# Kernel optimization log

Hardware: AMD Instinct MI355X
Metric: run time of the kernel (lower is better)

## Reference

```python
import jax, jax.numpy as jnp
import numpy as np

MAX_DEGREE = 7  # selected_degree for every neuron (== config.max_degree)


def _cheb_combine(alpha, coeffs):
    """sum_d coeffs[:, d] * T_d(alpha) via the Chebyshev recurrence.

    alpha:  [B, out]
    coeffs: [out, D+1]
    returns [B, out]
    """
    t_m2 = jnp.ones_like(alpha)          # T_0
    t_m1 = alpha                          # T_1
    acc = coeffs[:, 0] + coeffs[:, 1] * alpha

    def body(carry, c_d):                 # c_d: [out]
        tm2, tm1, a = carry
        t = 2.0 * alpha * tm1 - tm2       # T_d recurrence
        return (tm1, t, a + c_d * t), None

    (_, _, acc), _ = jax.lax.scan(body, (t_m2, t_m1, acc), coeffs[:, 2:].T)
    return acc


def _kan_layer(x, w, b, coeffs, cW, cb):
    # w: [out, in] (stacked per-neuron projection vectors), b: [out]
    alpha = x @ w.T + b                   # [B, out] -- per-neuron scalar projection
    neuron_out = _cheb_combine(alpha, coeffs)  # [B, out]
    return neuron_out @ cW + cb           # combine_W [out,out], combin_b [out]


def setup_inputs() -> dict:
    key = jax.random.key(0)
    ks = jax.random.split(key, 12)
    B = 16384
    shape = [1024, 1024, 256]
    D1 = MAX_DEGREE + 1
    inp = {"x": jax.random.normal(ks[0], (B, shape[0]), dtype=jnp.float32)}
    ki = 1
    for li, (din, dout) in enumerate(zip(shape[:-1], shape[1:]), start=1):
        inp[f"w{li}"] = jax.random.normal(ks[ki], (dout, din), dtype=jnp.float32) / np.sqrt(din); ki += 1
        inp[f"b{li}"] = jnp.zeros((dout,), dtype=jnp.float32)
        inp[f"coeffs{li}"] = jax.random.normal(ks[ki], (dout, D1), dtype=jnp.float32) * 0.1; ki += 1
        inp[f"cW{li}"] = jnp.eye(dout, dtype=jnp.float32)
        inp[f"cb{li}"] = jnp.zeros((dout,), dtype=jnp.float32)
    return inp


def reference(x, w1, b1, coeffs1, cW1, cb1, w2, b2, coeffs2, cW2, cb2):
    h = _kan_layer(x, w1, b1, coeffs1, cW1, cb1)
    return _kan_layer(h, w2, b2, coeffs2, cW2, cb2)
```

## Files before the change

kernel.cpp:

```cpp
#include <hip/hip_runtime.h>


typedef __attribute__((ext_vector_type(8))) short short8;
typedef __attribute__((ext_vector_type(4))) float f32x4;
typedef unsigned short ushort_t;

#define GAS(p) ((const __attribute__((address_space(1))) void*)(p))
#define LAS(p) ((__attribute__((address_space(3))) void*)(p))

__device__ __forceinline__ void split2(float f, ushort_t& h, ushort_t& l) {
    const unsigned u = __float_as_uint(f);
    h = (ushort_t)(u >> 16);
    const float hf = __uint_as_float(u & 0xFFFF0000u);
    l = (ushort_t)(__float_as_uint(f - hf) >> 16);
}

__global__ __launch_bounds__(256) void split_f32(const float* __restrict__ src,
                                                 ushort_t* __restrict__ hi,
                                                 ushort_t* __restrict__ lo, int n4) {
    const int i = blockIdx.x * 256 + threadIdx.x;
    if (i >= n4) return;
    const float4 v = ((const float4*)src)[i];
    ushort4 h, l;
    split2(v.x, h.x, l.x); split2(v.y, h.y, l.y);
    split2(v.z, h.z, l.z); split2(v.w, h.w, l.w);
    ((ushort4*)hi)[i] = h;
    ((ushort4*)lo)[i] = l;
}

__global__ __launch_bounds__(256) void bias2eff_kernel(const float* __restrict__ cb1,
                                                       const float* __restrict__ w2,
                                                       const float* __restrict__ b2,
                                                       float* __restrict__ out) {
    const int n = threadIdx.x;
    float s = 0.f;
    for (int k = 0; k < 1024; ++k) s = fmaf(cb1[k], w2[n * 1024 + k], s);
    out[n] = s + b2[n];
}

__global__ __launch_bounds__(256) void tsplit_kernel(const float* __restrict__ src,
                                                     ushort_t* __restrict__ hiT,
                                                     ushort_t* __restrict__ loT) {
    const int i = blockIdx.x * 256 + threadIdx.x;
    const int r = i >> 8, c = i & 255;
    ushort_t h, l;
    split2(src[r * 256 + c], h, l);
    hiT[c * 256 + r] = h;
    loT[c * 256 + r] = l;
}

constexpr int PKT = 16;
__global__ __launch_bounds__(256)
void prep_gemm_sk(const float* __restrict__ A, const float* __restrict__ W,
                  float* __restrict__ Cp, int M, int N, int K, int KS) {
    __shared__ float As[PKT][68];
    __shared__ float Bs[PKT][68];
    const int tid = threadIdx.x;
    const int bn = blockIdx.x, bm = blockIdx.y, bz = blockIdx.z;
    const int kc = K / KS, k0 = bz * kc;
    const int tx = tid & 15, ty = tid >> 4;
    float acc[4][4];
#pragma unroll
    for (int i = 0; i < 4; ++i)
#pragma unroll
        for (int j = 0; j < 4; ++j) acc[i][j] = 0.f;
    const float* Ab = A + (size_t)(bm * 64) * K + k0;
    const float* Wb = W + (size_t)(bn * 64) * K + k0;
    const int sr = tid >> 2;
    const int sc = (tid & 3) * 4;
    for (int kt = 0; kt < kc; kt += PKT) {
        const float4 va = *(const float4*)(Ab + (size_t)sr * K + kt + sc);
        As[sc + 0][sr] = va.x; As[sc + 1][sr] = va.y; As[sc + 2][sr] = va.z; As[sc + 3][sr] = va.w;
        const float4 vb = *(const float4*)(Wb + (size_t)sr * K + kt + sc);
        Bs[sc + 0][sr] = vb.x; Bs[sc + 1][sr] = vb.y; Bs[sc + 2][sr] = vb.z; Bs[sc + 3][sr] = vb.w;
        __syncthreads();
#pragma unroll
        for (int k = 0; k < PKT; ++k) {
            const float4 a4 = *(const float4*)&As[k][ty * 4];
            const float4 b4 = *(const float4*)&Bs[k][tx * 4];
            const float a[4] = {a4.x, a4.y, a4.z, a4.w};
            const float b[4] = {b4.x, b4.y, b4.z, b4.w};
#pragma unroll
            for (int i = 0; i < 4; ++i)
#pragma unroll
                for (int j = 0; j < 4; ++j) acc[i][j] = fmaf(a[i], b[j], acc[i][j]);
        }
        __syncthreads();
    }
    float* Cb = Cp + (size_t)bz * M * N + (size_t)(bm * 64 + ty * 4) * N + bn * 64 + tx * 4;
#pragma unroll
    for (int i = 0; i < 4; ++i)
        *(float4*)(Cb + (size_t)i * N) = make_float4(acc[i][0], acc[i][1], acc[i][2], acc[i][3]);
}

__global__ __launch_bounds__(256)
void combine_split(const float* __restrict__ Cp, ushort_t* __restrict__ hi,
                   ushort_t* __restrict__ lo, int n4, int KS) {
    const int i = blockIdx.x * 256 + threadIdx.x;
    if (i >= n4) return;
    float4 s = ((const float4*)Cp)[i];
    for (int z = 1; z < KS; ++z) {
        const float4 v = ((const float4*)Cp)[(size_t)z * n4 + i];
        s.x += v.x; s.y += v.y; s.z += v.z; s.w += v.w;
    }
    ushort4 h, l;
    split2(s.x, h.x, l.x); split2(s.y, h.y, l.y);
    split2(s.z, h.z, l.z); split2(s.w, h.w, l.w);
    ((ushort4*)hi)[i] = h;
    ((ushort4*)lo)[i] = l;
}

template<bool CHEB, bool OUT_F32>
__global__ __launch_bounds__(256)
void kan_mfma(const ushort_t* __restrict__ Ahg,
              const ushort_t* __restrict__ Alg,
              const ushort_t* __restrict__ Bhg,
              const ushort_t* __restrict__ Blg,
              const float* __restrict__ bias,
              const float* __restrict__ coeffs,
              float* __restrict__ Cf,
              ushort_t* __restrict__ Chh,
              ushort_t* __restrict__ Chl,
              int M, int N, int K)
{
    __shared__ __align__(16) ushort_t Ah[128 * 32];
    __shared__ __align__(16) ushort_t Al[128 * 32];
    __shared__ __align__(16) ushort_t Bh[128 * 32];
    __shared__ __align__(16) ushort_t Bl[128 * 32];

    const int tid  = threadIdx.x;
    const int lane = tid & 63;
    const int wave = tid >> 6;

    const int gx = gridDim.x;
    const int nwg = gx * gridDim.y;
    int wg = blockIdx.y * gx + blockIdx.x;
    wg = (wg & 7) * (nwg >> 3) + (wg >> 3);
    const int bn = wg % gx;
    const int bm = wg / gx;

    const int wm = wave >> 1, wn = wave & 1;
    const int lr = lane & 15;
    const int lg = lane >> 4;

    f32x4 acc[4][4];
#pragma unroll
    for (int m = 0; m < 4; ++m)
#pragma unroll
        for (int n = 0; n < 4; ++n) acc[m][n] = f32x4{0.f, 0.f, 0.f, 0.f};

    const size_t aRow0 = (size_t)(bm * 128);
    const size_t bRow0 = (size_t)(bn * 128);
    const int g = wave;
    const int ldsb = g * 1024;

    for (int kt = 0; kt < K; kt += 32) {
#pragma unroll
        for (int r0 = 0; r0 < 128; r0 += 64) {
            const size_t goA = (aRow0 + r0 + lane) * K + kt + g * 8;
            const size_t goB = (bRow0 + r0 + lane) * K + kt + g * 8;
            __builtin_amdgcn_global_load_lds(GAS(Ahg + goA), LAS(&Ah[ldsb + r0 * 8]), 16, 0, 0);
            __builtin_amdgcn_global_load_lds(GAS(Alg + goA), LAS(&Al[ldsb + r0 * 8]), 16, 0, 0);
            __builtin_amdgcn_global_load_lds(GAS(Bhg + goB), LAS(&Bh[ldsb + r0 * 8]), 16, 0, 0);
            __builtin_amdgcn_global_load_lds(GAS(Blg + goB), LAS(&Bl[ldsb + r0 * 8]), 16, 0, 0);
        }
        __syncthreads();

        short8 a_h[4], a_l[4], b_h[4], b_l[4];
#pragma unroll
        for (int m = 0; m < 4; ++m) {
            const int off = lg * 1024 + (wm * 64 + m * 16 + lr) * 8;
            a_h[m] = *(const short8*)&Ah[off];
            a_l[m] = *(const short8*)&Al[off];
        }
#pragma unroll
        for (int n = 0; n < 4; ++n) {
            const int off = lg * 1024 + (wn * 64 + n * 16 + lr) * 8;
            b_h[n] = *(const short8*)&Bh[off];
            b_l[n] = *(const short8*)&Bl[off];
        }
#pragma unroll
        for (int m = 0; m < 4; ++m)
#pragma unroll
            for (int n = 0; n < 4; ++n) {
                acc[m][n] = __builtin_amdgcn_mfma_f32_16x16x32_bf16(a_h[m], b_h[n], acc[m][n], 0, 0, 0);
                acc[m][n] = __builtin_amdgcn_mfma_f32_16x16x32_bf16(a_h[m], b_l[n], acc[m][n], 0, 0, 0);
                acc[m][n] = __builtin_amdgcn_mfma_f32_16x16x32_bf16(a_l[m], b_h[n], acc[m][n], 0, 0, 0);
            }
        __syncthreads();
    }

    const int gm0 = bm * 128 + wm * 64;
    const int gn0 = bn * 128 + wn * 64;
#pragma unroll
    for (int n = 0; n < 4; ++n) {
        const int colg = gn0 + n * 16 + lr;
        const float bia = bias[colg];
        float cf[8];
        if constexpr (CHEB) {
            const float4 u0 = *(const float4*)(coeffs + (size_t)colg * 8);
            const float4 u1 = *(const float4*)(coeffs + (size_t)colg * 8 + 4);
            cf[0] = u0.x; cf[1] = u0.y; cf[2] = u0.z; cf[3] = u0.w;
            cf[4] = u1.x; cf[5] = u1.y; cf[6] = u1.z; cf[7] = u1.w;
        }
#pragma unroll
        for (int m = 0; m < 4; ++m) {
            const int rowb = gm0 + m * 16 + lg * 4;
#pragma unroll
            for (int j = 0; j < 4; ++j) {
                const float alpha = acc[m][n][j] + bia;
                float v;
                if constexpr (CHEB) {
                    float tm2 = 1.f, tm1 = alpha;
                    v = fmaf(cf[1], alpha, cf[0]);
#pragma unroll
                    for (int d = 2; d < 8; ++d) {
                        const float t = 2.f * alpha * tm1 - tm2;
                        v = fmaf(cf[d], t, v);
                        tm2 = tm1; tm1 = t;
                    }
                } else {
                    v = alpha;
                }
                const size_t o = (size_t)(rowb + j) * N + colg;
                if constexpr (OUT_F32) {
                    Cf[o] = v;
                } else {
                    ushort_t h, l2;
                    split2(v, h, l2);
                    Chh[o] = h; Chl[o] = l2;
                }
            }
        }
    }
}

extern "C" void kernel_launch(void* const* d_in, const int* in_sizes, int n_in,
                              void* d_out, int out_size, void* d_ws, size_t ws_size,
                              hipStream_t stream) {
    const float* x       = (const float*)d_in[0];
    const float* w1      = (const float*)d_in[1];
    const float* b1      = (const float*)d_in[2];
    const float* coeffs1 = (const float*)d_in[3];
    const float* cW1     = (const float*)d_in[4];
    const float* cb1     = (const float*)d_in[5];
    const float* w2      = (const float*)d_in[6];
    const float* b2      = (const float*)d_in[7];
    const float* coeffs2 = (const float*)d_in[8];
    const float* cW2     = (const float*)d_in[9];
    const float* cb2     = (const float*)d_in[10];

    constexpr int B  = 16384;
    constexpr int D1 = 1024;
    constexpr int D2 = 256;
    constexpr int KS = 4;

    char* w = (char*)d_ws;
    size_t off = 0;
    auto alloc = [&](size_t bytes) { char* p = w + off; off += (bytes + 255) & ~(size_t)255; return p; };
    ushort_t* xh   = (ushort_t*)alloc((size_t)B * D1 * 2);
    ushort_t* xl   = (ushort_t*)alloc((size_t)B * D1 * 2);
    ushort_t* hh   = (ushort_t*)alloc((size_t)B * D1 * 2);
    ushort_t* hl   = (ushort_t*)alloc((size_t)B * D1 * 2);
    ushort_t* ph   = (ushort_t*)alloc((size_t)B * D2 * 2);
    ushort_t* pl   = (ushort_t*)alloc((size_t)B * D2 * 2);
    ushort_t* w1h  = (ushort_t*)alloc((size_t)D1 * D1 * 2);
    ushort_t* w1l  = (ushort_t*)alloc((size_t)D1 * D1 * 2);
    float*    m2p  = (float*)alloc((size_t)KS * D2 * D1 * 4);
    ushort_t* m2h  = (ushort_t*)alloc((size_t)D2 * D1 * 2);
    ushort_t* m2l  = (ushort_t*)alloc((size_t)D2 * D1 * 2);
    ushort_t* cw2h = (ushort_t*)alloc((size_t)D2 * D2 * 2);
    ushort_t* cw2l = (ushort_t*)alloc((size_t)D2 * D2 * 2);
    float*    b2e  = (float*)alloc(D2 * 4);

    split_f32<<<dim3(B * D1 / 4 / 256), dim3(256), 0, stream>>>(x, xh, xl, B * D1 / 4);
    split_f32<<<dim3(D1 * D1 / 4 / 256), dim3(256), 0, stream>>>(w1, w1h, w1l, D1 * D1 / 4);
    prep_gemm_sk<<<dim3(D1 / 64, D2 / 64, KS), dim3(256), 0, stream>>>(w2, cW1, m2p, D2, D1, D1, KS);
    combine_split<<<dim3(D2 * D1 / 4 / 256), dim3(256), 0, stream>>>(m2p, m2h, m2l, D2 * D1 / 4, KS);
    bias2eff_kernel<<<dim3(1), dim3(256), 0, stream>>>(cb1, w2, b2, b2e);
    tsplit_kernel<<<dim3(D2 * D2 / 256), dim3(256), 0, stream>>>(cW2, cw2h, cw2l);

    kan_mfma<true, false><<<dim3(D1 / 128, B / 128), dim3(256), 0, stream>>>(
        xh, xl, w1h, w1l, b1, coeffs1, nullptr, hh, hl, B, D1, D1);
    kan_mfma<true, false><<<dim3(D2 / 128, B / 128), dim3(256), 0, stream>>>(
        hh, hl, m2h, m2l, b2e, coeffs2, nullptr, ph, pl, B, D2, D1);
    kan_mfma<false, true><<<dim3(D2 / 128, B / 128), dim3(256), 0, stream>>>(
        ph, pl, cw2h, cw2l, cb2, nullptr, (float*)d_out, nullptr, nullptr, B, D2, D2);
}
```

Before: 417.3 us.

## Add 256x256-tile MFMA kernel for layer-1 GEMM and parallelize bias prep

```diff
diff --git a/kernel.cpp b/kernel.cpp
--- a/kernel.cpp
+++ b/kernel.cpp
@@ -32,10 +32,20 @@
                                                        const float* __restrict__ w2,
                                                        const float* __restrict__ b2,
                                                        float* __restrict__ out) {
-    const int n = threadIdx.x;
+    const int wave = threadIdx.x >> 6, lane = threadIdx.x & 63;
+    const int n = blockIdx.x * 4 + wave;
+    const float4* row = (const float4*)(w2 + (size_t)n * 1024);
+    const float4* c4  = (const float4*)cb1;
     float s = 0.f;
-    for (int k = 0; k < 1024; ++k) s = fmaf(cb1[k], w2[n * 1024 + k], s);
-    out[n] = s + b2[n];
+#pragma unroll
+    for (int i = 0; i < 4; ++i) {
+        const int idx = lane + i * 64;
+        const float4 a = row[idx], c = c4[idx];
+        s += a.x * c.x + a.y * c.y + a.z * c.z + a.w * c.w;
+    }
+#pragma unroll
+    for (int off = 32; off; off >>= 1) s += __shfl_down(s, off);
+    if (lane == 0) out[n] = s + b2[n];
 }
 
 __global__ __launch_bounds__(256) void tsplit_kernel(const float* __restrict__ src,
@@ -108,6 +118,149 @@
     split2(s.z, h.z, l.z); split2(s.w, h.w, l.w);
     ((ushort4*)hi)[i] = h;
     ((ushort4*)lo)[i] = l;
+}
+
+__global__ __launch_bounds__(512, 2)
+void kan_mfma256(const ushort_t* __restrict__ Ahg,
+                 const ushort_t* __restrict__ Alg,
+                 const ushort_t* __restrict__ Bhg,
+                 const ushort_t* __restrict__ Blg,
+                 const float* __restrict__ bias,
+                 const float* __restrict__ coeffs,
+                 ushort_t* __restrict__ Chh,
+                 ushort_t* __restrict__ Chl,
+                 int M, int N, int K)
+{
+    __shared__ __align__(16) ushort_t LDS[2][4][256 * 32];
+
+    const int tid  = threadIdx.x;
+    const int lane = tid & 63;
+    const int wave = tid >> 6;
+
+    const int gx  = gridDim.x;
+    const int nwg = gx * gridDim.y;
+    int wg = blockIdx.y * gx + blockIdx.x;
+    wg = (wg & 7) * (nwg >> 3) + (wg >> 3);
+    const int bn = wg % gx;
+    const int bm = wg / gx;
+
+    const int wm = wave >> 2;
+    const int wn = wave & 3;
+    const int lr = lane & 15;
+    const int lg = lane >> 4;
+
+    const int sg  = wave & 3;
+    const int r0a = (wave >> 2) * 128;
+    const size_t aRow0 = (size_t)bm * 256;
+    const size_t bRow0 = (size_t)bn * 256;
+
+    f32x4 acc[8][4];
+#pragma unroll
+    for (int m = 0; m < 8; ++m)
+#pragma unroll
+        for (int n = 0; n < 4; ++n) acc[m][n] = f32x4{0.f, 0.f, 0.f, 0.f};
+
+    auto stage = [&](int q, int s, int kt) {
+        const int r0 = r0a + ((q & 1) ? 64 : 0);
+        const int lo = (q >= 2) ? 1 : 0;
+        const size_t ga = (aRow0 + r0 + lane) * K + kt + sg * 8;
+        const size_t gb = (bRow0 + r0 + lane) * K + kt + sg * 8;
+        const int di = sg * 2048 + r0 * 8;
+        __builtin_amdgcn_global_load_lds(GAS((lo ? Alg : Ahg) + ga),
+                                         LAS(&LDS[s][lo][di]), 16, 0, 0);
+        __builtin_amdgcn_global_load_lds(GAS((lo ? Blg : Bhg) + gb),
+                                         LAS(&LDS[s][2 + lo][di]), 16, 0, 0);
+    };
+
+#pragma unroll
+    for (int q = 0; q < 4; ++q) stage(q, 0, 0);
+    asm volatile("s_waitcnt vmcnt(0)" ::: "memory");
+    __builtin_amdgcn_s_barrier();
+
+    const int nt = K >> 5;
+    constexpr int MH[4] = {0, 1, 1, 0};
+    constexpr int NH[4] = {0, 0, 1, 1};
+
+    for (int t = 0; t < nt; ++t) {
+        const int cur = t & 1;
+        const int kt_next = (t + 1) << 5;
+        const bool more = (t + 1) < nt;
+
+#pragma unroll
+        for (int q = 0; q < 4; ++q) {
+            const int mh = MH[q], nh = NH[q];
+            short8 ah[4], al4[4], bh2[2], bl2[2];
+#pragma unroll
+            for (int m = 0; m < 4; ++m) {
+                const int idx = lg * 2048 + (wm * 128 + (mh * 4 + m) * 16 + lr) * 8;
+                ah[m]  = *(const short8*)&LDS[cur][0][idx];
+                al4[m] = *(const short8*)&LDS[cur][1][idx];
+            }
+#pragma unroll
+            for (int n = 0; n < 2; ++n) {
+                const int idx = lg * 2048 + (wn * 64 + (nh * 2 + n) * 16 + lr) * 8;
+                bh2[n] = *(const short8*)&LDS[cur][2][idx];
+                bl2[n] = *(const short8*)&LDS[cur][3][idx];
+            }
+            if (more) stage(q, cur ^ 1, kt_next);
+
+            __builtin_amdgcn_s_barrier();
+            asm volatile("s_waitcnt lgkmcnt(0)" ::: "memory");
+            __builtin_amdgcn_sched_barrier(0);
+            __builtin_amdgcn_s_setprio(1);
+#pragma unroll
+            for (int m = 0; m < 4; ++m)
+#pragma unroll
+                for (int n = 0; n < 2; ++n) {
+                    const int am = mh * 4 + m, an = nh * 2 + n;
+                    acc[am][an] = __builtin_amdgcn_mfma_f32_16x16x32_bf16(ah[m],  bh2[n], acc[am][an], 0, 0, 0);
+                    acc[am][an] = __builtin_amdgcn_mfma_f32_16x16x32_bf16(ah[m],  bl2[n], acc[am][an], 0, 0, 0);
+                    acc[am][an] = __builtin_amdgcn_mfma_f32_16x16x32_bf16(al4[m], bh2[n], acc[am][an], 0, 0, 0);
+                }
+            __builtin_amdgcn_s_setprio(0);
+            __builtin_amdgcn_s_barrier();
+        }
+
+        if (more) {
+            asm volatile("s_waitcnt vmcnt(0)" ::: "memory");
+            __builtin_amdgcn_s_barrier();
+        }
+    }
+
+    const int gm0 = bm * 256 + wm * 128;
+    const int gn0 = bn * 256 + wn * 64;
+#pragma unroll
+    for (int n = 0; n < 4; ++n) {
+        const int colg = gn0 + n * 16 + lr;
+        const float bia = bias[colg];
+        float cf[8];
+        {
+            const float4 u0 = *(const float4*)(coeffs + (size_t)colg * 8);
+            const float4 u1 = *(const float4*)(coeffs + (size_t)colg * 8 + 4);
+            cf[0] = u0.x; cf[1] = u0.y; cf[2] = u0.z; cf[3] = u0.w;
+            cf[4] = u1.x; cf[5] = u1.y; cf[6] = u1.z; cf[7] = u1.w;
+        }
+#pragma unroll
+        for (int m = 0; m < 8; ++m) {
+            const int rowb = gm0 + m * 16 + lg * 4;
+#pragma unroll
+            for (int j = 0; j < 4; ++j) {
+                const float alpha = acc[m][n][j] + bia;
+                float tm2 = 1.f, tm1 = alpha;
+                float v = fmaf(cf[1], alpha, cf[0]);
+#pragma unroll
+                for (int d = 2; d < 8; ++d) {
+                    const float tch = 2.f * alpha * tm1 - tm2;
+                    v = fmaf(cf[d], tch, v);
+                    tm2 = tm1; tm1 = tch;
+                }
+                const size_t o = (size_t)(rowb + j) * N + colg;
+                ushort_t h, l2;
+                split2(v, h, l2);
+                Chh[o] = h; Chl[o] = l2;
+            }
+        }
+    }
 }
 
 template<bool CHEB, bool OUT_F32>
@@ -277,11 +430,11 @@
     split_f32<<<dim3(D1 * D1 / 4 / 256), dim3(256), 0, stream>>>(w1, w1h, w1l, D1 * D1 / 4);
     prep_gemm_sk<<<dim3(D1 / 64, D2 / 64, KS), dim3(256), 0, stream>>>(w2, cW1, m2p, D2, D1, D1, KS);
     combine_split<<<dim3(D2 * D1 / 4 / 256), dim3(256), 0, stream>>>(m2p, m2h, m2l, D2 * D1 / 4, KS);
-    bias2eff_kernel<<<dim3(1), dim3(256), 0, stream>>>(cb1, w2, b2, b2e);
+    bias2eff_kernel<<<dim3(D2 / 4), dim3(256), 0, stream>>>(cb1, w2, b2, b2e);
     tsplit_kernel<<<dim3(D2 * D2 / 256), dim3(256), 0, stream>>>(cW2, cw2h, cw2l);
 
-    kan_mfma<true, false><<<dim3(D1 / 128, B / 128), dim3(256), 0, stream>>>(
-        xh, xl, w1h, w1l, b1, coeffs1, nullptr, hh, hl, B, D1, D1);
+    kan_mfma256<<<dim3(D1 / 256, B / 256), dim3(512), 0, stream>>>(
+        xh, xl, w1h, w1l, b1, coeffs1, hh, hl, B, D1, D1);
     kan_mfma<true, false><<<dim3(D2 / 128, B / 128), dim3(256), 0, stream>>>(
         hh, hl, m2h, m2l, b2e, coeffs2, nullptr, ph, pl, B, D2, D1);
     kan_mfma<false, true><<<dim3(D2 / 128, B / 128), dim3(256), 0, stream>>>(
```

Result: faster. 355.0 us (-14.9%).
